# Optimization experiments

Hardware: AMD Instinct MI355X
Metric: run time of the kernel (lower is better)

The kernel has to match this reference:

```python
import math
import jax, jax.numpy as jnp
import numpy as np
from jax import lax

PATCHSIZE = [(8, 8), (4, 4), (2, 2), (1, 1)]  # (width, height)
BN_EPS = 1e-5


def setup_inputs() -> dict:
    key = jax.random.key(0)
    ks = jax.random.split(key, 6)
    b, c, h, w = 4, 256, 64, 64
    s = 1.0 / math.sqrt(c)
    return {
        "x": jax.random.normal(ks[0], (b, c, h, w), jnp.float32),
        "Wq": jax.random.normal(ks[1], (c, c), jnp.float32) * s,
        "bq": jnp.zeros((c,), jnp.float32),
        "Wk": jax.random.normal(ks[2], (c, c), jnp.float32) * s,
        "bk": jnp.zeros((c,), jnp.float32),
        "Wv": jax.random.normal(ks[3], (c, c), jnp.float32) * s,
        "bv": jnp.zeros((c,), jnp.float32),
        "Wo": jax.random.normal(ks[4], (c, c, 3, 3), jnp.float32) * (1.0 / math.sqrt(c * 9)),
        "bo": jnp.zeros((c,), jnp.float32),
        "gamma": jnp.ones((c,), jnp.float32),
        "beta": jnp.zeros((c,), jnp.float32),
        "running_mean": jnp.zeros((c,), jnp.float32),
        "running_var": jnp.ones((c,), jnp.float32),
    }


def _patch_attention(q, k, v, ph, pw):
    # q/k/v: [b, dk, h, w] -> tokens [b, n_patches, dk*ph*pw]
    b, dk, h, w = q.shape
    oh, ow = h // ph, w // pw

    def to_tok(t):
        t = t.reshape(b, dk, oh, ph, ow, pw)
        return t.transpose(0, 2, 4, 1, 3, 5).reshape(b, oh * ow, dk * ph * pw)

    qt, kt, vt = to_tok(q), to_tok(k), to_tok(v)
    scale = 1.0 / math.sqrt(dk * ph * pw)
    scores = jnp.einsum("bnd,bmd->bnm", qt, kt) * scale
    y = jnp.einsum("bnm,bmd->bnd", jax.nn.softmax(scores, axis=-1), vt)
    y = y.reshape(b, oh, ow, dk, ph, pw).transpose(0, 3, 1, 4, 2, 5)
    return y.reshape(b, dk, h, w)


def reference(x, Wq, bq, Wk, bk, Wv, bv, Wo, bo, gamma, beta, running_mean, running_var):
    b, c, h, w = x.shape
    nh = len(PATCHSIZE)
    dk = c // nh
    # 1x1 conv QKV projections
    q = jnp.einsum("bchw,oc->bohw", x, Wq) + bq[:, None, None]
    k = jnp.einsum("bchw,oc->bohw", x, Wk) + bk[:, None, None]
    v = jnp.einsum("bchw,oc->bohw", x, Wv) + bv[:, None, None]
    outs = []
    for i, (pw_, ph_) in enumerate(PATCHSIZE):
        sl = slice(i * dk, (i + 1) * dk)
        outs.append(_patch_attention(q[:, sl], k[:, sl], v[:, sl], ph_, pw_))
    out = jnp.concatenate(outs, axis=1)
    # 3x3 conv, SAME padding
    out = lax.conv_general_dilated(
        out, Wo, window_strides=(1, 1), padding="SAME",
        dimension_numbers=("NCHW", "OIHW", "NCHW"),
    ) + bo[:, None, None]
    # BatchNorm2d (inference-mode with running stats)
    inv = lax.rsqrt(running_var + BN_EPS)
    out = (out - running_mean[:, None, None]) * (gamma * inv)[:, None, None] + beta[:, None, None]
    # LeakyReLU(0.2)
    return jnp.where(out >= 0, out, 0.2 * out)
```

## Files before the change

### kernel.cpp

```cpp
#include <hip/hip_runtime.h>
#include <hip/hip_bf16.h>
#include <math.h>

#define NPOS 4096
#define CPB  1048576
#define QOFF  ((size_t)0)
#define KOFF  ((size_t)4194304)
#define VOFF  ((size_t)8388608)
#define AOFF  ((size_t)12582912)
#define S0OFF ((size_t)16777216)
#define WTOFF ((size_t)21250048)
#define QTOFF   S0OFF
#define KTOFF   (S0OFF + (size_t)2097152)
#define SP0OFF  (S0OFF + (size_t)4194304)
#define VTOFF   QOFF
#define ML3OFF  (QOFF + (size_t)2097152)
#define ML2OFF  (QOFF + (size_t)2228224)
#define OP3OFF  KOFF
#define SP1OFF  VOFF
#define OP2OFF  (VOFF + (size_t)2097152)

#define LOG2E 1.44269504088896340736f

typedef __attribute__((ext_vector_type(8))) short bf16x8;
typedef __attribute__((ext_vector_type(4))) float f32x4;

static __device__ __forceinline__ unsigned short f2bf(float f) {
  __hip_bfloat16 h = __float2bfloat16(f);
  unsigned short u;
  __builtin_memcpy(&u, &h, sizeof(u));
  return u;
}

__global__ __launch_bounds__(256) void qkv_wo(
    const float* __restrict__ x,
    const float* __restrict__ Wq, const float* __restrict__ Wk, const float* __restrict__ Wv,
    const float* __restrict__ bq, const float* __restrict__ bk, const float* __restrict__ bv,
    const float* __restrict__ Wo, unsigned short* __restrict__ W2,
    float* __restrict__ ws) {
  if (blockIdx.z == 12) {
    int o = blockIdx.y * 64 + blockIdx.x;
    size_t base = (size_t)o * 2304;
#pragma unroll
    for (int r = 0; r < 9; ++r) {
      int rr = r * 256 + threadIdx.x;
      int c = rr / 9, k = rr % 9;
      W2[(size_t)k * 65536 + (size_t)o * 256 + c] = f2bf(Wo[base + rr]);
    }
    return;
  }
  int b = blockIdx.z / 3, t = blockIdx.z % 3;
  const float* W    = (t == 0) ? Wq : (t == 1) ? Wk : Wv;
  const float* bias = (t == 0) ? bq : (t == 1) ? bk : bv;
  float* outp = ws + (size_t)t * 4194304 + (size_t)b * CPB;
  int o0 = blockIdx.y * 64, p0 = blockIdx.x * 64;
  __shared__ unsigned short Wt[64 * 72];
  __shared__ unsigned short Xs[64 * 72];
  int tid = threadIdx.x;
  int wv = tid >> 6, l = tid & 63;
  int lg = l >> 4, ll = l & 15;
  f32x4 acc[4];
#pragma unroll
  for (int mi = 0; mi < 4; ++mi) acc[mi] = (f32x4){0.f, 0.f, 0.f, 0.f};

  int wol = tid >> 2, wcp = (tid & 3) * 16;
  int xcc = tid >> 6, xpz = tid & 63;

  for (int c0 = 0; c0 < 256; c0 += 64) {
    __syncthreads();
#pragma unroll
    for (int u = 0; u < 4; ++u) {
      float4 w4 = *(const float4*)&W[(size_t)(o0 + wol) * 256 + c0 + wcp + u * 4];
      ushort4 pk;
      pk.x = f2bf(w4.x); pk.y = f2bf(w4.y); pk.z = f2bf(w4.z); pk.w = f2bf(w4.w);
      *(ushort4*)&Wt[wol * 72 + wcp + u * 4] = pk;
    }
#pragma unroll
    for (int r = 0; r < 16; ++r) {
      int c = xcc * 16 + r;
      Xs[xpz * 72 + c] = f2bf(x[(size_t)b * CPB + (size_t)(c0 + c) * NPOS + p0 + xpz]);
    }
    __syncthreads();
#pragma unroll
    for (int ks = 0; ks < 2; ++ks) {
      bf16x8 xb = *(const bf16x8*)&Xs[(wv * 16 + ll) * 72 + ks * 32 + lg * 8];
#pragma unroll
      for (int mi = 0; mi < 4; ++mi) {
        bf16x8 wa = *(const bf16x8*)&Wt[(mi * 16 + ll) * 72 + ks * 32 + lg * 8];
        acc[mi] = __builtin_amdgcn_mfma_f32_16x16x32_bf16(wa, xb, acc[mi], 0, 0, 0);
      }
    }
  }
#pragma unroll
  for (int mi = 0; mi < 4; ++mi)
#pragma unroll
    for (int r = 0; r < 4; ++r) {
      int o = o0 + mi * 16 + lg * 4 + r;
      outp[(size_t)o * NPOS + p0 + wv * 16 + ll] = acc[mi][r] + bias[o];
    }
}

template<int PH, int PW, int HEAD>
__device__ __forceinline__ void qk_body(const float* __restrict__ srcbase,
                                        unsigned short* __restrict__ dstbase) {
  constexpr int PP = PH * PW, D = 64 * PP, OW = 64 / PW;
  int b = blockIdx.y;
  const float* src = srcbase + (size_t)b * CPB + (size_t)HEAD * 64 * NPOS;
  unsigned short* dst = dstbase + ((size_t)b * 4 + HEAD) * 262144;
  int idx = blockIdx.x * 256 + threadIdx.x;
  int t = idx / (D / 8), j8 = idx % (D / 8);
  int po = t / OW, qo = t % OW;
  union { unsigned short u16[8]; uint4 v; } pk;
#pragma unroll
  for (int e = 0; e < 8; ++e) {
    int d = j8 * 8 + e;
    int c = d / PP, rem = d % PP, y = rem / PW, x = rem % PW;
    pk.u16[e] = f2bf(src[(size_t)c * NPOS + (po * PH + y) * 64 + qo * PW + x]);
  }
  *(uint4*)&dst[(size_t)t * D + j8 * 8] = pk.v;
}

template<int PH, int PW, int HEAD>
__device__ __forceinline__ void v_body(const float* __restrict__ vsrc,
                                       unsigned short* __restrict__ vt) {
  constexpr int PP = PH * PW, NT = NPOS / PP, OW = 64 / PW;
  int b = blockIdx.y;
  const float* src = vsrc + (size_t)b * CPB + (size_t)HEAD * 64 * NPOS;
  unsigned short* dst = vt + ((size_t)b * 4 + HEAD) * 262144;
  int idx = blockIdx.x * 256 + threadIdx.x;
  int d = idx / (NT / 8), j8 = idx % (NT / 8);
  int c = d / PP, rem = d % PP, y = rem / PW, x = rem % PW;
  union { unsigned short u16[8]; uint4 v; } pk;
#pragma unroll
  for (int e = 0; e < 8; ++e) {
    int t = j8 * 8 + e;
    int po = t / OW, qo = t % OW;
    pk.u16[e] = f2bf(src[(size_t)c * NPOS + (po * PH + y) * 64 + qo * PW + x]);
  }
  *(uint4*)&dst[(size_t)d * NT + j8 * 8] = pk.v;
}

__device__ __forceinline__ void qk3_body(const float* __restrict__ srcbase,
                                         unsigned short* __restrict__ dstbase,
                                         float (*tile)[65]) {
  int pt = blockIdx.x, b = blockIdx.y;
  const float* src = srcbase + (size_t)b * CPB + (size_t)192 * NPOS + pt * 64;
  unsigned short* dst = dstbase + ((size_t)b * 4 + 3) * 262144 + (size_t)pt * 4096;
  int tid = threadIdx.x;
  int a = tid >> 6, pz = tid & 63;
#pragma unroll
  for (int r = 0; r < 16; ++r) {
    int ch = a + r * 4;
    tile[pz][ch] = src[(size_t)ch * NPOS + pz];
  }
  __syncthreads();
  int ch2 = tid & 63, pr = tid >> 6;
#pragma unroll
  for (int r = 0; r < 16; ++r) {
    int pos = pr + r * 4;
    dst[(size_t)pos * 64 + ch2] = f2bf(tile[pos][ch2]);
  }
}

__global__ __launch_bounds__(256) void prep_qk_all(const float* __restrict__ qf32,
                                                   const float* __restrict__ kf32,
                                                   unsigned short* __restrict__ qt,
                                                   unsigned short* __restrict__ kt_) {
  __shared__ float tile[64][65];
  switch (blockIdx.z) {
    case 0:  qk_body<8, 8, 0>(qf32, qt);  break;
    case 1:  qk_body<8, 8, 0>(kf32, kt_); break;
    case 2:  qk_body<4, 4, 1>(qf32, qt);  break;
    case 3:  qk_body<4, 4, 1>(kf32, kt_); break;
    case 4:  qk_body<2, 2, 2>(qf32, qt);  break;
    case 5:  qk_body<2, 2, 2>(kf32, kt_); break;
    case 6:  if (blockIdx.x < 64) qk3_body(qf32, qt, tile);  break;
    default: if (blockIdx.x < 64) qk3_body(kf32, kt_, tile); break;
  }
}

__global__ __launch_bounds__(256) void prep_v_all(const float* __restrict__ vf32,
                                                  unsigned short* __restrict__ vt) {
  switch (blockIdx.z) {
    case 0:  v_body<8, 8, 0>(vf32, vt); break;
    case 1:  v_body<4, 4, 1>(vf32, vt); break;
    case 2:  v_body<2, 2, 2>(vf32, vt); break;
    default: v_body<1, 1, 3>(vf32, vt); break;
  }
}

template<int NTOK, int DDIM, int NSPLIT, int KVB, int PH, int PW, int HEAD>
__device__ __forceinline__ void flash_body(
    unsigned char* smem, int b, int q0, int split,
    const unsigned short* __restrict__ qt, const unsigned short* __restrict__ kt_,
    const unsigned short* __restrict__ vt, float* __restrict__ opart,
    float* __restrict__ ml, unsigned short* __restrict__ attbf) {
  constexpr int KSTR = DDIM + 8;
  constexpr int VSTR = KVB + 8;
  constexpr int NT   = KVB / 16;
  constexpr int KCH  = DDIM / 32;
  constexpr int PKS  = KVB / 32;
  constexpr int OCG  = DDIM / 16;
  constexpr float scale = (DDIM == 64) ? 0.125f : (DDIM == 256) ? 0.0625f
                        : (DDIM == 1024) ? 0.03125f : 0.015625f;
  constexpr float SC2 = scale * LOG2E;
  constexpr int PP = PH * PW, OW = 64 / PW;
  const unsigned short* Q = qt + ((size_t)b * 4 + HEAD) * 262144;
  const unsigned short* K = kt_ + ((size_t)b * 4 + HEAD) * 262144;
  const unsigned short* V = vt + ((size_t)b * 4 + HEAD) * 262144;
  unsigned short* Ks = (unsigned short*)smem;
  unsigned short* Vs = Ks + KVB * KSTR;
  unsigned short* Psw = Vs + DDIM * VSTR;
  int tid = threadIdx.x;
  int wv = tid >> 6, l = tid & 63;
  int lg = l >> 4, ll = l & 15;
  int qw = q0 + wv * 16;
  unsigned short* Ps = Psw + wv * 16 * VSTR;

  bf16x8 qf[KCH];
#pragma unroll
  for (int kc = 0; kc < KCH; ++kc)
    qf[kc] = *(const bf16x8*)&Q[(size_t)(qw + ll) * DDIM + kc * 32 + lg * 8];

  bf16x8 onesf;
#pragma unroll
  for (int e = 0; e < 8; ++e) onesf[e] = (short)0x3F80;

  f32x4 lacc = (f32x4){0.f, 0.f, 0.f, 0.f};
  f32x4 o_acc[OCG];
#pragma unroll
  for (int c = 0; c < OCG; ++c) o_acc[c] = (f32x4){0.f, 0.f, 0.f, 0.f};

  for (int kt0 = split * (NTOK / NSPLIT); kt0 < (split + 1) * (NTOK / NSPLIT); kt0 += KVB) {
    __syncthreads();
#pragma unroll
    for (int i = 0; i < KVB * DDIM / 2048; ++i) {
      int u = i * 256 + tid;
      int key = u / (DDIM / 8), part = u % (DDIM / 8);
      *(uint4*)&Ks[key * KSTR + part * 8] =
          *(const uint4*)&K[(size_t)(kt0 + key) * DDIM + part * 8];
    }
#pragma unroll
    for (int i = 0; i < KVB * DDIM / 2048; ++i) {
      int u = i * 256 + tid;
      int d = u / (KVB / 8), part = u % (KVB / 8);
      *(uint4*)&Vs[d * VSTR + part * 8] =
          *(const uint4*)&V[(size_t)d * NTOK + kt0 + part * 8];
    }
    __syncthreads();
    f32x4 s_acc[NT];
#pragma unroll
    for (int n = 0; n < NT; ++n) s_acc[n] = (f32x4){0.f, 0.f, 0.f, 0.f};
#pragma unroll
    for (int n = 0; n < NT; ++n)
#pragma unroll
      for (int kc = 0; kc < KCH; ++kc) {
        bf16x8 kf = *(const bf16x8*)&Ks[(n * 16 + ll) * KSTR + kc * 32 + lg * 8];
        s_acc[n] = __builtin_amdgcn_mfma_f32_16x16x32_bf16(qf[kc], kf, s_acc[n], 0, 0, 0);
      }
#pragma unroll
    for (int n = 0; n < NT; ++n)
#pragma unroll
      for (int r = 0; r < 4; ++r) {
        float p = exp2f(fminf(s_acc[n][r] * SC2, 80.f));
        Ps[(lg * 4 + r) * VSTR + n * 16 + ll] = f2bf(p);
      }
#pragma unroll
    for (int pk = 0; pk < PKS; ++pk) {
      bf16x8 pa = *(const bf16x8*)&Ps[ll * VSTR + pk * 32 + lg * 8];
      lacc = __builtin_amdgcn_mfma_f32_16x16x32_bf16(pa, onesf, lacc, 0, 0, 0);
#pragma unroll
      for (int c = 0; c < OCG; ++c) {
        bf16x8 vf = *(const bf16x8*)&Vs[(c * 16 + ll) * VSTR + pk * 32 + lg * 8];
        o_acc[c] = __builtin_amdgcn_mfma_f32_16x16x32_bf16(pa, vf, o_acc[c], 0, 0, 0);
      }
    }
  }
  if constexpr (NSPLIT > 1) {
    size_t ob = (size_t)(b * NSPLIT + split) * NTOK;
#pragma unroll
    for (int r = 0; r < 4; ++r) {
      int q = qw + lg * 4 + r;
#pragma unroll
      for (int c = 0; c < OCG; ++c)
        opart[(ob + q) * DDIM + c * 16 + ll] = o_acc[c][r];
      if (ll == 0) {
        ml[(ob + q) * 2]     = 0.f;
        ml[(ob + q) * 2 + 1] = lacc[r];
      }
    }
  } else {
#pragma unroll
    for (int r = 0; r < 4; ++r) {
      float inv = 1.0f / lacc[r];
      int q = qw + lg * 4 + r;
      int po = q / OW, qo = q % OW;
#pragma unroll
      for (int c = 0; c < OCG; ++c) {
        int d = c * 16 + ll;
        int ch = d / PP, rem = d % PP, y = rem / PW, x = rem % PW;
        int pos = (po * PH + y) * 64 + qo * PW + x;
        attbf[((size_t)b * NPOS + pos) * 256 + HEAD * 64 + ch] = f2bf(o_acc[c][r] * inv);
      }
    }
  }
}

__device__ __forceinline__ void h0_score_body(unsigned char* smem, int b, int ds,
                                              const unsigned short* __restrict__ qt,
                                              const unsigned short* __restrict__ kt_,
                                              float* __restrict__ spart) {
  const unsigned short* Q = qt + ((size_t)b * 4 + 0) * 262144;
  const unsigned short* K = kt_ + ((size_t)b * 4 + 0) * 262144;
  unsigned short* Qc = (unsigned short*)smem;
  unsigned short* Kc = Qc + 64 * 72;
  int tid = threadIdx.x;
  int wv = tid >> 6, l = tid & 63;
  int lg = l >> 4, ll = l & 15;
  f32x4 s_acc[4];
#pragma unroll
  for (int n = 0; n < 4; ++n) s_acc[n] = (f32x4){0.f, 0.f, 0.f, 0.f};
  for (int ch = 0; ch < 8; ++ch) {
    int d0 = ds * 512 + ch * 64;
    __syncthreads();
#pragma unroll
    for (int i = 0; i < 2; ++i) {
      int u = i * 256 + tid, row = u >> 3, part = u & 7;
      *(uint4*)&Qc[row * 72 + part * 8] = *(const uint4*)&Q[(size_t)row * 4096 + d0 + part * 8];
      *(uint4*)&Kc[row * 72 + part * 8] = *(const uint4*)&K[(size_t)row * 4096 + d0 + part * 8];
    }
    __syncthreads();
#pragma unroll
    for (int n = 0; n < 4; ++n)
#pragma unroll
      for (int ks = 0; ks < 2; ++ks) {
        bf16x8 qa = *(const bf16x8*)&Qc[(wv * 16 + ll) * 72 + ks * 32 + lg * 8];
        bf16x8 kf = *(const bf16x8*)&Kc[(n * 16 + ll) * 72 + ks * 32 + lg * 8];
        s_acc[n] = __builtin_amdgcn_mfma_f32_16x16x32_bf16(qa, kf, s_acc[n], 0, 0, 0);
      }
  }
#pragma unroll
  for (int n = 0; n < 4; ++n)
#pragma unroll
    for (int r = 0; r < 4; ++r)
      spart[(((size_t)b * 8 + ds) * 64 + (wv * 16 + lg * 4 + r)) * 64 + n * 16 + ll] =
          s_acc[n][r];
}

__device__ __forceinline__ void h1_score_body(unsigned char* smem, int b, int qtile, int ds,
                                              const unsigned short* __restrict__ qt,
                                              const unsigned short* __restrict__ kt_,
                                              float* __restrict__ spart) {
  int q0 = qtile * 64, dbase = ds * 128;
  const unsigned short* Q = qt + ((size_t)b * 4 + 1) * 262144;
  const unsigned short* K = kt_ + ((size_t)b * 4 + 1) * 262144;
  unsigned short* Qc = (unsigned short*)smem;
  unsigned short* Kc = Qc + 64 * 72;
  int tid = threadIdx.x;
  int wv = tid >> 6, l = tid & 63;
  int lg = l >> 4, ll = l & 15;
  f32x4 s_acc[16];
#pragma unroll
  for (int n = 0; n < 16; ++n) s_acc[n] = (f32x4){0.f, 0.f, 0.f, 0.f};
  for (int dc = 0; dc < 2; ++dc) {
    int d0 = dbase + dc * 64;
    __syncthreads();
#pragma unroll
    for (int i = 0; i < 2; ++i) {
      int u = i * 256 + tid, row = u >> 3, part = u & 7;
      *(uint4*)&Qc[row * 72 + part * 8] =
          *(const uint4*)&Q[(size_t)(q0 + row) * 1024 + d0 + part * 8];
    }
#pragma unroll
    for (int i = 0; i < 8; ++i) {
      int u = i * 256 + tid, row = u >> 3, part = u & 7;
      *(uint4*)&Kc[row * 72 + part * 8] =
          *(const uint4*)&K[(size_t)row * 1024 + d0 + part * 8];
    }
    __syncthreads();
#pragma unroll
    for (int ks = 0; ks < 2; ++ks) {
      bf16x8 qa = *(const bf16x8*)&Qc[(wv * 16 + ll) * 72 + ks * 32 + lg * 8];
#pragma unroll
      for (int n = 0; n < 16; ++n) {
        bf16x8 kf = *(const bf16x8*)&Kc[(n * 16 + ll) * 72 + ks * 32 + lg * 8];
        s_acc[n] = __builtin_amdgcn_mfma_f32_16x16x32_bf16(qa, kf, s_acc[n], 0, 0, 0);
      }
    }
  }
#pragma unroll
  for (int n = 0; n < 16; ++n)
#pragma unroll
    for (int r = 0; r < 4; ++r) {
      int q = q0 + wv * 16 + lg * 4 + r;
      spart[(((size_t)b * 8 + ds) * 256 + q) * 256 + n * 16 + ll] = s_acc[n][r];
    }
}

__global__ __launch_bounds__(256) void attn_all(
    const unsigned short* __restrict__ qt, const unsigned short* __restrict__ kt_,
    const unsigned short* __restrict__ vt,
    float* __restrict__ op2, float* __restrict__ ml2,
    float* __restrict__ op3, float* __restrict__ ml3,
    float* __restrict__ sp0, float* __restrict__ sp1,
    unsigned short* __restrict__ attbf) {
  __shared__ __align__(16) unsigned char smem[46080];
  int bid = blockIdx.x;
  if (bid < 1024) {
    int b = bid & 3, qy = (bid >> 2) & 63, split = bid >> 8;
    flash_body<4096, 64, 4, 64, 1, 1, 3>(smem, b, qy * 64, split, qt, kt_, vt,
                                         op3, ml3, attbf);
  } else if (bid < 1152) {
    int r = bid - 1024;
    int b = r & 3, qy = (r >> 2) & 15, split = r >> 6;
    flash_body<1024, 256, 2, 32, 2, 2, 2>(smem, b, qy * 64, split, qt, kt_, vt,
                                          op2, ml2, attbf);
  } else {
    int r = bid - 1152;
    if (r < 32) h0_score_body(smem, r >> 3, r & 7, qt, kt_, sp0);
    else {
      int rr = r - 32;
      h1_score_body(smem, rr >> 5, (rr >> 3) & 3, rr & 7, qt, kt_, sp1);
    }
  }
}

__device__ __forceinline__ void h0_pv_body(unsigned char* smem, int b, int ds,
                                           const float* __restrict__ spart,
                                           const unsigned short* __restrict__ vt,
                                           unsigned short* __restrict__ attbf) {
  const unsigned short* V = vt + ((size_t)b * 4 + 0) * 262144;
  float* S = (float*)smem;
  unsigned short* Ps = (unsigned short*)(smem + 16640);
  unsigned short* Vc = Ps + 64 * 72;
  int tid = threadIdx.x;
  int wv = tid >> 6, l = tid & 63;
  int lg = l >> 4, ll = l & 15;
#pragma unroll
  for (int i = 0; i < 16; ++i) {
    int idx = i * 256 + tid, q = idx >> 6, k = idx & 63;
    float s = 0.f;
#pragma unroll
    for (int sl = 0; sl < 8; ++sl)
      s += spart[(((size_t)b * 8 + sl) * 64 + q) * 64 + k];
    S[q * 65 + k] = s;
  }
  __syncthreads();
  for (int rr = 0; rr < 16; ++rr) {
    int row = wv * 16 + rr;
    float v = S[row * 65 + l] * 0.015625f;
    float m = v;
#pragma unroll
    for (int d = 32; d >= 1; d >>= 1) m = fmaxf(m, __shfl_xor(m, d));
    float p = __expf(v - m);
    float su = p;
#pragma unroll
    for (int d = 32; d >= 1; d >>= 1) su += __shfl_xor(su, d);
    Ps[row * 72 + l] = f2bf(p / su);
  }
  __syncthreads();
  for (int ch = 0; ch < 8; ++ch) {
    int d0 = ds * 512 + ch * 64;
    __syncthreads();
#pragma unroll
    for (int i = 0; i < 2; ++i) {
      int u = i * 256 + tid, row = u >> 3, part = u & 7;
      *(uint4*)&Vc[row * 72 + part * 8] =
          *(const uint4*)&V[(size_t)(d0 + row) * 64 + part * 8];
    }
    __syncthreads();
    f32x4 o[4];
#pragma unroll
    for (int cg = 0; cg < 4; ++cg) o[cg] = (f32x4){0.f, 0.f, 0.f, 0.f};
#pragma unroll
    for (int cg = 0; cg < 4; ++cg)
#pragma unroll
      for (int ks = 0; ks < 2; ++ks) {
        bf16x8 pa = *(const bf16x8*)&Ps[(wv * 16 + ll) * 72 + ks * 32 + lg * 8];
        bf16x8 vf = *(const bf16x8*)&Vc[(cg * 16 + ll) * 72 + ks * 32 + lg * 8];
        o[cg] = __builtin_amdgcn_mfma_f32_16x16x32_bf16(pa, vf, o[cg], 0, 0, 0);
      }
#pragma unroll
    for (int cg = 0; cg < 4; ++cg)
#pragma unroll
      for (int r = 0; r < 4; ++r) {
        int q = wv * 16 + lg * 4 + r;
        int d = d0 + cg * 16 + ll;
        int c = d >> 6, rem = d & 63, y = rem >> 3, x = rem & 7;
        int po = q >> 3, qo = q & 7;
        int pos = (po * 8 + y) * 64 + qo * 8 + x;
        attbf[((size_t)b * NPOS + pos) * 256 + c] = f2bf(o[cg][r]);
      }
  }
}

__device__ __forceinline__ void h1_pv_body(unsigned char* smem, int b, int qtile, int vs,
                                           const float* __restrict__ spart,
                                           const unsigned short* __restrict__ vt,
                                           unsigned short* __restrict__ attbf) {
  int q0 = qtile * 64, dv0 = vs * 128;
  const unsigned short* V = vt + ((size_t)b * 4 + 1) * 262144;
  unsigned short* Ps = (unsigned short*)smem;
  unsigned short* Vs = Ps + 64 * 264;
  int tid = threadIdx.x;
  int wv = tid >> 6, l = tid & 63;
  int lg = l >> 4, ll = l & 15;
  for (int rr = 0; rr < 16; ++rr) {
    int row = q0 + wv * 16 + rr;
    float sv[4];
#pragma unroll
    for (int c4 = 0; c4 < 4; ++c4) {
      float s = 0.f;
#pragma unroll
      for (int sl = 0; sl < 8; ++sl)
        s += spart[(((size_t)b * 8 + sl) * 256 + row) * 256 + c4 * 64 + l];
      sv[c4] = s * 0.03125f;
    }
    float m = fmaxf(fmaxf(sv[0], sv[1]), fmaxf(sv[2], sv[3]));
#pragma unroll
    for (int d = 32; d >= 1; d >>= 1) m = fmaxf(m, __shfl_xor(m, d));
    float p[4], su = 0.f;
#pragma unroll
    for (int c4 = 0; c4 < 4; ++c4) { p[c4] = __expf(sv[c4] - m); su += p[c4]; }
#pragma unroll
    for (int d = 32; d >= 1; d >>= 1) su += __shfl_xor(su, d);
    float inv = 1.0f / su;
#pragma unroll
    for (int c4 = 0; c4 < 4; ++c4)
      Ps[(wv * 16 + rr) * 264 + c4 * 64 + l] = f2bf(p[c4] * inv);
  }
  for (int vc = 0; vc < 4; ++vc) {
    int d0 = dv0 + vc * 32;
    __syncthreads();
#pragma unroll
    for (int i = 0; i < 4; ++i) {
      int u = i * 256 + tid, row = u >> 5, part = u & 31;
      *(uint4*)&Vs[row * 264 + part * 8] =
          *(const uint4*)&V[(size_t)(d0 + row) * 256 + part * 8];
    }
    __syncthreads();
    f32x4 o[2];
    o[0] = (f32x4){0.f, 0.f, 0.f, 0.f};
    o[1] = (f32x4){0.f, 0.f, 0.f, 0.f};
#pragma unroll
    for (int ks = 0; ks < 8; ++ks) {
      bf16x8 pa = *(const bf16x8*)&Ps[(wv * 16 + ll) * 264 + ks * 32 + lg * 8];
#pragma unroll
      for (int cg = 0; cg < 2; ++cg) {
        bf16x8 vf = *(const bf16x8*)&Vs[(cg * 16 + ll) * 264 + ks * 32 + lg * 8];
        o[cg] = __builtin_amdgcn_mfma_f32_16x16x32_bf16(pa, vf, o[cg], 0, 0, 0);
      }
    }
#pragma unroll
    for (int cg = 0; cg < 2; ++cg)
#pragma unroll
      for (int r = 0; r < 4; ++r) {
        int q = q0 + wv * 16 + lg * 4 + r;
        int d = d0 + cg * 16 + ll;
        int c = d >> 4, rem = d & 15, y = rem >> 2, x = rem & 3;
        int po = q >> 4, qo = q & 15;
        int pos = (po * 4 + y) * 64 + qo * 4 + x;
        attbf[((size_t)b * NPOS + pos) * 256 + 64 + c] = f2bf(o[cg][r]);
      }
  }
}

__global__ __launch_bounds__(256) void finish_all(
    const float* __restrict__ sp0, const float* __restrict__ sp1,
    const float* __restrict__ op2, const float* __restrict__ ml2,
    const float* __restrict__ op3, const float* __restrict__ ml3,
    const unsigned short* __restrict__ vt, unsigned short* __restrict__ attbf) {
  __shared__ __align__(16) unsigned char smem[50688];
  int bid = blockIdx.x;
  if (bid < 32) { h0_pv_body(smem, bid >> 3, bid & 7, sp0, vt, attbf); return; }
  if (bid < 160) {
    int r = bid - 32;
    h1_pv_body(smem, r >> 5, (r >> 3) & 3, r & 7, sp1, vt, attbf);
    return;
  }
  int cb = bid - 160;
  if (cb < 4096) {
    int b = cb >> 10, q = cb & 1023;
    int d = threadIdx.x;
    float num = 0.f, den = 0.f;
#pragma unroll
    for (int s = 0; s < 2; ++s) {
      den += ml2[((size_t)(b * 2 + s) * 1024 + q) * 2 + 1];
      num += op2[((size_t)(b * 2 + s) * 1024 + q) * 256 + d];
    }
    int c = d >> 2, rem = d & 3, y = rem >> 1, x = rem & 1;
    int po = q >> 5, qo = q & 31;
    int pos = (po * 2 + y) * 64 + qo * 2 + x;
    attbf[((size_t)b * NPOS + pos) * 256 + 128 + c] = f2bf(num / den);
  } else {
    cb -= 4096;
    int b = cb >> 10, qt4 = cb & 1023;
    int q = qt4 * 4 + (threadIdx.x >> 6), ch = threadIdx.x & 63;
    float num = 0.f, den = 0.f;
#pragma unroll
    for (int s = 0; s < 4; ++s) {
      den += ml3[((size_t)(b * 4 + s) * 4096 + q) * 2 + 1];
      num += op3[((size_t)(b * 4 + s) * 4096 + q) * 64 + ch];
    }
    attbf[((size_t)b * 4096 + q) * 256 + 192 + ch] = f2bf(num / den);
  }
}

__global__ __launch_bounds__(256) void conv_mfma(
    const unsigned short* __restrict__ attbf, const unsigned short* __restrict__ w2,
    const float* __restrict__ bo, const float* __restrict__ gamma,
    const float* __restrict__ beta, const float* __restrict__ rmean,
    const float* __restrict__ rvar, float* __restrict__ out) {
  int hp = blockIdx.x, ot = blockIdx.y, b = blockIdx.z;
  int h0 = hp * 2, o0 = ot * 64;
  __shared__ unsigned short As[2 * 66 * 72];
  __shared__ unsigned short Ws[3 * 64 * 72];
  int tid = threadIdx.x;
  int wi = tid >> 6, l = tid & 63;
  int hrow = wi >> 1, wseg = wi & 1;
  int lg = l >> 4, ll = l & 15;
  const size_t attb = (size_t)b * NPOS * 256;
  f32x4 acc[4][2];
#pragma unroll
  for (int mi = 0; mi < 4; ++mi)
#pragma unroll
    for (int ni = 0; ni < 2; ++ni) acc[mi][ni] = (f32x4){0.f, 0.f, 0.f, 0.f};

  for (int dy = 0; dy < 3; ++dy) {
    for (int c0 = 0; c0 < 256; c0 += 64) {
      __syncthreads();
      if (tid < 128) {
        int rowl = tid >> 6, w = tid & 63;
        int ghh = h0 + dy - 1 + rowl;
        uint4 z = make_uint4(0u, 0u, 0u, 0u);
        uint4 a[8];
        if (ghh >= 0 && ghh < 64) {
          const uint4* src = (const uint4*)(attbf + attb + ((size_t)(ghh * 64 + w) * 256 + c0));
#pragma unroll
          for (int q = 0; q < 8; ++q) a[q] = src[q];
        } else {
#pragma unroll
          for (int q = 0; q < 8; ++q) a[q] = z;
        }
        uint4* dst = (uint4*)&As[(rowl * 66 + 1 + w) * 72];
#pragma unroll
        for (int q = 0; q < 8; ++q) dst[q] = a[q];
        if (w == 0 || w == 63) {
          uint4* dz = (uint4*)&As[(rowl * 66 + ((w == 0) ? 0 : 65)) * 72];
#pragma unroll
          for (int q = 0; q < 8; ++q) dz[q] = z;
        }
      }
      if (tid >= 64) {
        int p = tid - 64;
        int dx = p >> 6, ol = p & 63;
        const uint4* src = (const uint4*)(w2 + ((size_t)(dy * 3 + dx) * 65536 +
                                                (size_t)(o0 + ol) * 256 + c0));
        uint4* dst = (uint4*)&Ws[(dx * 64 + ol) * 72];
#pragma unroll
        for (int q = 0; q < 8; ++q) dst[q] = src[q];
      }
      __syncthreads();
#pragma unroll
      for (int dx = 0; dx < 3; ++dx) {
#pragma unroll
        for (int ks = 0; ks < 2; ++ks) {
          bf16x8 af[4];
#pragma unroll
          for (int mi = 0; mi < 4; ++mi)
            af[mi] = *(const bf16x8*)&Ws[(dx * 64 + mi * 16 + ll) * 72 + ks * 32 + lg * 8];
#pragma unroll
          for (int ni = 0; ni < 2; ++ni) {
            bf16x8 bfr = *(const bf16x8*)&As[(hrow * 66 + wseg * 32 + ni * 16 + ll + dx) * 72 +
                                             ks * 32 + lg * 8];
#pragma unroll
            for (int mi = 0; mi < 4; ++mi)
              acc[mi][ni] = __builtin_amdgcn_mfma_f32_16x16x32_bf16(af[mi], bfr, acc[mi][ni],
                                                                    0, 0, 0);
          }
        }
      }
    }
  }
  int h = h0 + hrow;
#pragma unroll
  for (int mi = 0; mi < 4; ++mi) {
#pragma unroll
    for (int r = 0; r < 4; ++r) {
      int o = o0 + mi * 16 + lg * 4 + r;
      float g  = gamma[o] * rsqrtf(rvar[o] + 1e-5f);
      float bb = (bo[o] - rmean[o]) * g + beta[o];
#pragma unroll
      for (int ni = 0; ni < 2; ++ni) {
        float zv = acc[mi][ni][r] * g + bb;
        zv = (zv >= 0.f) ? zv : 0.2f * zv;
        out[((size_t)(b * 256 + o)) * NPOS + h * 64 + wseg * 32 + ni * 16 + ll] = zv;
      }
    }
  }
}

extern "C" void kernel_launch(void* const* d_in, const int* in_sizes, int n_in,
                              void* d_out, int out_size, void* d_ws, size_t ws_size,
                              hipStream_t stream) {
  (void)in_sizes; (void)n_in; (void)out_size; (void)ws_size;
  const float* x     = (const float*)d_in[0];
  const float* Wq    = (const float*)d_in[1];
  const float* bq    = (const float*)d_in[2];
  const float* Wk    = (const float*)d_in[3];
  const float* bk    = (const float*)d_in[4];
  const float* Wv    = (const float*)d_in[5];
  const float* bv    = (const float*)d_in[6];
  const float* Wo    = (const float*)d_in[7];
  const float* bo    = (const float*)d_in[8];
  const float* gamma = (const float*)d_in[9];
  const float* beta  = (const float*)d_in[10];
  const float* rmean = (const float*)d_in[11];
  const float* rvar  = (const float*)d_in[12];
  float* ws  = (float*)d_ws;
  float* out = (float*)d_out;
  unsigned short* attbf = (unsigned short*)(ws + AOFF);
  unsigned short* w2bf  = (unsigned short*)(ws + WTOFF);
  unsigned short* qt    = (unsigned short*)(ws + QTOFF);
  unsigned short* kt    = (unsigned short*)(ws + KTOFF);
  unsigned short* vt    = (unsigned short*)(ws + VTOFF);
  const float* qf32 = ws + QOFF;
  const float* kf32 = ws + KOFF;
  const float* vf32 = ws + VOFF;

  qkv_wo<<<dim3(64, 4, 13), 256, 0, stream>>>(x, Wq, Wk, Wv, bq, bk, bv, Wo, w2bf, ws);

  prep_qk_all<<<dim3(128, 4, 8), 256, 0, stream>>>(qf32, kf32, qt, kt);
  prep_v_all<<<dim3(128, 4, 4), 256, 0, stream>>>(vf32, vt);

  attn_all<<<1312, 256, 0, stream>>>(qt, kt, vt,
                                     ws + OP2OFF, ws + ML2OFF,
                                     ws + OP3OFF, ws + ML3OFF,
                                     ws + SP0OFF, ws + SP1OFF, attbf);

  finish_all<<<8352, 256, 0, stream>>>(ws + SP0OFF, ws + SP1OFF,
                                       ws + OP2OFF, ws + ML2OFF,
                                       ws + OP3OFF, ws + ML3OFF, vt, attbf);

  conv_mfma<<<dim3(32, 4, 4), 256, 0, stream>>>(attbf, w2bf, bo, gamma, beta,
                                                rmean, rvar, out);
}
```

Baseline: 213.4 us.

## Fuse QKV projection with patch-token layout scatter into bf16 buffers

The QKV projection kernel now converts its accumulators to bf16 in shared memory and scatters them directly into the per-head patch-token layouts (Q/K token-major, V transposed) that attention consumes. This removes the fp32 Q/K/V intermediate writes and the two separate prep kernels that re-read and rearranged them, saving two launches and a full fp32 round-trip through global memory. Each block maps to one head and one image row, so the scatter uses small vector stores, and for the 1x1 V head only one wave writes.

```diff
diff --git a/kernel.cpp b/kernel.cpp
--- a/kernel.cpp
+++ b/kernel.cpp
@@ -32,12 +32,61 @@
   return u;
 }
 
-__global__ __launch_bounds__(256) void qkv_wo(
+template<int PH, int PW>
+__device__ __forceinline__ void scat_qk(unsigned short* __restrict__ dst,
+                                        const unsigned short* __restrict__ Ac,
+                                        int gh, int tid) {
+  constexpr int PP = PH * PW, OW = 64 / PW, D = 64 * PP;
+  int po = gh / PH, y = gh % PH;
+  constexpr int NCH = 64 * OW;
+#pragma unroll
+  for (int j = 0; j < NCH / 256; ++j) {
+    int id = j * 256 + tid;
+    int c = id / OW, qo = id % OW;
+    int tt = po * OW + qo;
+    unsigned short buf[PW];
+#pragma unroll
+    for (int x = 0; x < PW; ++x) buf[x] = Ac[c * 66 + qo * PW + x];
+    unsigned short* dp = &dst[(size_t)tt * D + c * PP + y * PW];
+    if constexpr (PW == 8)      { uint4 v;  __builtin_memcpy(&v, buf, 16); *(uint4*)dp = v; }
+    else if constexpr (PW == 4) { uint2 v;  __builtin_memcpy(&v, buf, 8);  *(uint2*)dp = v; }
+    else                        { unsigned v; __builtin_memcpy(&v, buf, 4); *(unsigned*)dp = v; }
+  }
+}
+
+template<int PH, int PW>
+__device__ __forceinline__ void scat_v(unsigned short* __restrict__ dst,
+                                       const unsigned short* __restrict__ Ac,
+                                       int gh, int tid) {
+  constexpr int PP = PH * PW, OW = 64 / PW, NT = 4096 / PP;
+  int po = gh / PH, y = gh % PH;
+  constexpr int NCH = 64 * PW;
+  constexpr int CPT = (NCH + 255) / 256;
+#pragma unroll
+  for (int j = 0; j < CPT; ++j) {
+    int id = j * 256 + tid;
+    if (NCH < 256 && id >= NCH) break;
+    int c = id / PW, x = id % PW;
+    int d = c * PP + y * PW + x;
+    unsigned short* dp = &dst[(size_t)d * NT + po * OW];
+#pragma unroll
+    for (int s = 0; s < OW; s += 8) {
+      unsigned short buf[8];
+#pragma unroll
+      for (int e = 0; e < 8; ++e) buf[e] = Ac[c * 66 + (s + e) * PW + x];
+      uint4 v; __builtin_memcpy(&v, buf, 16);
+      *(uint4*)&dp[s] = v;
+    }
+  }
+}
+
+__global__ __launch_bounds__(256) void qkv_fused(
     const float* __restrict__ x,
     const float* __restrict__ Wq, const float* __restrict__ Wk, const float* __restrict__ Wv,
     const float* __restrict__ bq, const float* __restrict__ bk, const float* __restrict__ bv,
     const float* __restrict__ Wo, unsigned short* __restrict__ W2,
-    float* __restrict__ ws) {
+    unsigned short* __restrict__ qt, unsigned short* __restrict__ kt_,
+    unsigned short* __restrict__ vt) {
   if (blockIdx.z == 12) {
     int o = blockIdx.y * 64 + blockIdx.x;
     size_t base = (size_t)o * 2304;
@@ -52,10 +101,11 @@
   int b = blockIdx.z / 3, t = blockIdx.z % 3;
   const float* W    = (t == 0) ? Wq : (t == 1) ? Wk : Wv;
   const float* bias = (t == 0) ? bq : (t == 1) ? bk : bv;
-  float* outp = ws + (size_t)t * 4194304 + (size_t)b * CPB;
-  int o0 = blockIdx.y * 64, p0 = blockIdx.x * 64;
-  __shared__ unsigned short Wt[64 * 72];
-  __shared__ unsigned short Xs[64 * 72];
+  int h = blockIdx.y, gh = blockIdx.x;
+  int o0 = h * 64, p0 = gh * 64;
+  __shared__ unsigned short smem[2 * 64 * 72];
+  unsigned short* Wt = smem;
+  unsigned short* Xs = smem + 64 * 72;
   int tid = threadIdx.x;
   int wv = tid >> 6, l = tid & 63;
   int lg = l >> 4, ll = l & 15;
@@ -91,101 +141,53 @@
       }
     }
   }
+  __syncthreads();
+  unsigned short* Ac = smem;
 #pragma unroll
   for (int mi = 0; mi < 4; ++mi)
 #pragma unroll
     for (int r = 0; r < 4; ++r) {
-      int o = o0 + mi * 16 + lg * 4 + r;
-      outp[(size_t)o * NPOS + p0 + wv * 16 + ll] = acc[mi][r] + bias[o];
-    }
-}
-
-template<int PH, int PW, int HEAD>
-__device__ __forceinline__ void qk_body(const float* __restrict__ srcbase,
-                                        unsigned short* __restrict__ dstbase) {
-  constexpr int PP = PH * PW, D = 64 * PP, OW = 64 / PW;
-  int b = blockIdx.y;
-  const float* src = srcbase + (size_t)b * CPB + (size_t)HEAD * 64 * NPOS;
-  unsigned short* dst = dstbase + ((size_t)b * 4 + HEAD) * 262144;
-  int idx = blockIdx.x * 256 + threadIdx.x;
-  int t = idx / (D / 8), j8 = idx % (D / 8);
-  int po = t / OW, qo = t % OW;
-  union { unsigned short u16[8]; uint4 v; } pk;
-#pragma unroll
-  for (int e = 0; e < 8; ++e) {
-    int d = j8 * 8 + e;
-    int c = d / PP, rem = d % PP, y = rem / PW, x = rem % PW;
-    pk.u16[e] = f2bf(src[(size_t)c * NPOS + (po * PH + y) * 64 + qo * PW + x]);
-  }
-  *(uint4*)&dst[(size_t)t * D + j8 * 8] = pk.v;
-}
-
-template<int PH, int PW, int HEAD>
-__device__ __forceinline__ void v_body(const float* __restrict__ vsrc,
-                                       unsigned short* __restrict__ vt) {
-  constexpr int PP = PH * PW, NT = NPOS / PP, OW = 64 / PW;
-  int b = blockIdx.y;
-  const float* src = vsrc + (size_t)b * CPB + (size_t)HEAD * 64 * NPOS;
-  unsigned short* dst = vt + ((size_t)b * 4 + HEAD) * 262144;
-  int idx = blockIdx.x * 256 + threadIdx.x;
-  int d = idx / (NT / 8), j8 = idx % (NT / 8);
-  int c = d / PP, rem = d % PP, y = rem / PW, x = rem % PW;
-  union { unsigned short u16[8]; uint4 v; } pk;
-#pragma unroll
-  for (int e = 0; e < 8; ++e) {
-    int t = j8 * 8 + e;
-    int po = t / OW, qo = t % OW;
-    pk.u16[e] = f2bf(src[(size_t)c * NPOS + (po * PH + y) * 64 + qo * PW + x]);
-  }
-  *(uint4*)&dst[(size_t)d * NT + j8 * 8] = pk.v;
-}
-
-__device__ __forceinline__ void qk3_body(const float* __restrict__ srcbase,
-                                         unsigned short* __restrict__ dstbase,
-                                         float (*tile)[65]) {
-  int pt = blockIdx.x, b = blockIdx.y;
-  const float* src = srcbase + (size_t)b * CPB + (size_t)192 * NPOS + pt * 64;
-  unsigned short* dst = dstbase + ((size_t)b * 4 + 3) * 262144 + (size_t)pt * 4096;
-  int tid = threadIdx.x;
-  int a = tid >> 6, pz = tid & 63;
-#pragma unroll
-  for (int r = 0; r < 16; ++r) {
-    int ch = a + r * 4;
-    tile[pz][ch] = src[(size_t)ch * NPOS + pz];
-  }
+      int ol = mi * 16 + lg * 4 + r;
+      Ac[ol * 66 + wv * 16 + ll] = f2bf(acc[mi][r] + bias[o0 + ol]);
+    }
   __syncthreads();
-  int ch2 = tid & 63, pr = tid >> 6;
-#pragma unroll
-  for (int r = 0; r < 16; ++r) {
-    int pos = pr + r * 4;
-    dst[(size_t)pos * 64 + ch2] = f2bf(tile[pos][ch2]);
-  }
-}
-
-__global__ __launch_bounds__(256) void prep_qk_all(const float* __restrict__ qf32,
-                                                   const float* __restrict__ kf32,
-                                                   unsigned short* __restrict__ qt,
-                                                   unsigned short* __restrict__ kt_) {
-  __shared__ float tile[64][65];
-  switch (blockIdx.z) {
-    case 0:  qk_body<8, 8, 0>(qf32, qt);  break;
-    case 1:  qk_body<8, 8, 0>(kf32, kt_); break;
-    case 2:  qk_body<4, 4, 1>(qf32, qt);  break;
-    case 3:  qk_body<4, 4, 1>(kf32, kt_); break;
-    case 4:  qk_body<2, 2, 2>(qf32, qt);  break;
-    case 5:  qk_body<2, 2, 2>(kf32, kt_); break;
-    case 6:  if (blockIdx.x < 64) qk3_body(qf32, qt, tile);  break;
-    default: if (blockIdx.x < 64) qk3_body(kf32, kt_, tile); break;
-  }
-}
-
-__global__ __launch_bounds__(256) void prep_v_all(const float* __restrict__ vf32,
-                                                  unsigned short* __restrict__ vt) {
-  switch (blockIdx.z) {
-    case 0:  v_body<8, 8, 0>(vf32, vt); break;
-    case 1:  v_body<4, 4, 1>(vf32, vt); break;
-    case 2:  v_body<2, 2, 2>(vf32, vt); break;
-    default: v_body<1, 1, 3>(vf32, vt); break;
+  if (t < 2) {
+    unsigned short* dst = (t == 0 ? qt : kt_) + ((size_t)b * 4 + h) * 262144;
+    switch (h) {
+      case 0: scat_qk<8, 8>(dst, Ac, gh, tid); break;
+      case 1: scat_qk<4, 4>(dst, Ac, gh, tid); break;
+      case 2: scat_qk<2, 2>(dst, Ac, gh, tid); break;
+      default: {
+        int p = tid >> 2, c0 = (tid & 3) * 16;
+        unsigned short buf[16];
+#pragma unroll
+        for (int e = 0; e < 16; ++e) buf[e] = Ac[(c0 + e) * 66 + p];
+        uint4 v0, v1;
+        __builtin_memcpy(&v0, buf, 16);
+        __builtin_memcpy(&v1, buf + 8, 16);
+        uint4* d4 = (uint4*)&dst[(size_t)(gh * 64 + p) * 64 + c0];
+        d4[0] = v0; d4[1] = v1;
+      } break;
+    }
+  } else {
+    unsigned short* dst = vt + ((size_t)b * 4 + h) * 262144;
+    switch (h) {
+      case 0: scat_v<8, 8>(dst, Ac, gh, tid); break;
+      case 1: scat_v<4, 4>(dst, Ac, gh, tid); break;
+      case 2: scat_v<2, 2>(dst, Ac, gh, tid); break;
+      default: {
+        if (tid < 64) {
+#pragma unroll
+          for (int seg = 0; seg < 8; ++seg) {
+            unsigned short buf[8];
+#pragma unroll
+            for (int e = 0; e < 8; ++e) buf[e] = Ac[tid * 66 + seg * 8 + e];
+            uint4 v; __builtin_memcpy(&v, buf, 16);
+            *(uint4*)&dst[(size_t)tid * 4096 + gh * 64 + seg * 8] = v;
+          }
+        }
+      } break;
+    }
   }
 }
 
@@ -724,14 +726,9 @@
   unsigned short* qt    = (unsigned short*)(ws + QTOFF);
   unsigned short* kt    = (unsigned short*)(ws + KTOFF);
   unsigned short* vt    = (unsigned short*)(ws + VTOFF);
-  const float* qf32 = ws + QOFF;
-  const float* kf32 = ws + KOFF;
-  const float* vf32 = ws + VOFF;
-
-  qkv_wo<<<dim3(64, 4, 13), 256, 0, stream>>>(x, Wq, Wk, Wv, bq, bk, bv, Wo, w2bf, ws);
-
-  prep_qk_all<<<dim3(128, 4, 8), 256, 0, stream>>>(qf32, kf32, qt, kt);
-  prep_v_all<<<dim3(128, 4, 4), 256, 0, stream>>>(vf32, vt);
+
+  qkv_fused<<<dim3(64, 4, 13), 256, 0, stream>>>(x, Wq, Wk, Wv, bq, bk, bv,
+                                                 Wo, w2bf, qt, kt, vt);
 
   attn_all<<<1312, 256, 0, stream>>>(qt, kt, vt,
                                      ws + OP2OFF, ws + ML2OFF,
```

Measured after the change: 189.1 us. 11.4% less time.
